# Optimization experiments

Hardware: AMD Instinct MI355X
Metric: run time of the kernel (lower is better)

## Reference

```python
import jax, jax.numpy as jnp
import numpy as np
import math

B, N, D, H = 32, 512, 512, 8
DK = D // H
MAX_DIST = 100.0
BINS = 20
BIN_SIZE = MAX_DIST / BINS


def setup_inputs() -> dict:
    key = jax.random.key(0)
    ks = jax.random.split(key, 12)
    s = 1.0 / math.sqrt(D)
    inp = {
        "x": jax.random.normal(ks[0], (B, N, D), dtype=jnp.float32),
        "distance_matrix": jax.random.uniform(ks[1], (B, N, N), dtype=jnp.float32) * MAX_DIST,
        "Wq": jax.random.uniform(ks[2], (D, D), jnp.float32, -s, s),
        "bq": jax.random.uniform(ks[3], (D,), jnp.float32, -s, s),
        "Wk": jax.random.uniform(ks[4], (D, D), jnp.float32, -s, s),
        "bk": jax.random.uniform(ks[5], (D,), jnp.float32, -s, s),
        "Wv": jax.random.uniform(ks[6], (D, D), jnp.float32, -s, s),
        "bv": jax.random.uniform(ks[7], (D,), jnp.float32, -s, s),
        "Wo": jax.random.uniform(ks[8], (D, D), jnp.float32, -s, s),
        "bo": jax.random.uniform(ks[9], (D,), jnp.float32, -s, s),
        "dist_weights": jnp.ones((BINS + 1,), dtype=jnp.float32),
    }
    return inp


def reference(x, distance_matrix, Wq, bq, Wk, bk, Wv, bv, Wo, bo, dist_weights):
    temperature = 1.0
    # Linear projections; torch nn.Linear computes x @ W.T + b
    q = (x @ Wq.T + bq).reshape(B, N, H, DK).transpose(0, 2, 1, 3)  # [B,H,N,DK]
    k = (x @ Wk.T + bk).reshape(B, N, H, DK).transpose(0, 2, 1, 3)
    v = (x @ Wv.T + bv).reshape(B, N, H, DK).transpose(0, 2, 1, 3)

    scores = jnp.einsum("bhqd,bhkd->bhqk", q, k) / math.sqrt(DK)  # [B,H,N,N]

    # Relative position bias: bin distances, look up scalar weight per pair
    binned = jnp.clip((distance_matrix / BIN_SIZE).astype(jnp.int32), 0, BINS)  # [B,N,N]
    bias = dist_weights[binned] / temperature  # [B,N,N]
    scores = scores + bias[:, None, :, :]  # broadcast over heads

    attn = jax.nn.softmax(scores, axis=-1)  # dropout is identity in eval
    out = jnp.einsum("bhqk,bhkd->bhqd", attn, v)  # [B,H,N,DK]
    out = out.transpose(0, 2, 1, 3).reshape(B, N, D)
    return out @ Wo.T + bo
```

## Files before the change

kernel.cpp:

```cpp
#include <hip/hip_runtime.h>
#include <hip/hip_fp16.h>
#include <math.h>
#include <stdint.h>

#define BB 32
#define NN 512
#define DDIM 512
#define HH 8
#define DK 64

typedef __attribute__((ext_vector_type(8))) short short8;
typedef __attribute__((ext_vector_type(8))) _Float16 half8;
typedef __attribute__((ext_vector_type(2))) _Float16 half2v;
typedef __attribute__((ext_vector_type(4))) float floatx4;
typedef __attribute__((ext_vector_type(16))) float floatx16;
typedef unsigned short ushort_t;
typedef unsigned int uint_t;

__device__ __forceinline__ void gl_lds16(const void* g, void* l) {
    __builtin_amdgcn_global_load_lds(
        (const __attribute__((address_space(1))) uint_t*)g,
        (__attribute__((address_space(3))) uint_t*)l,
        16, 0, 0);
}

__device__ __forceinline__ ushort_t f2bf(float f) {
    uint_t u = __builtin_bit_cast(uint_t, f);
    u += 0x7fff + ((u >> 16) & 1);
    return (ushort_t)(u >> 16);
}

__device__ __forceinline__ uint_t pkbf(float a, float b) {
    return (uint_t)f2bf(a) | ((uint_t)f2bf(b) << 16);
}

__device__ __forceinline__ uint_t pkh(float a, float b) {
    return __builtin_bit_cast(uint_t, __builtin_amdgcn_cvt_pkrtz(a, b));
}

__device__ __forceinline__ float h2f(ushort_t u) {
    return __half2float(__ushort_as_half(u));
}

__global__ __launch_bounds__(256) void cvt_bf16(const float* __restrict__ s,
                                                ushort_t* __restrict__ d, int n8) {
    const int i = blockIdx.x * 256 + threadIdx.x;
    if (i >= n8) return;
    const float4 a = ((const float4*)s)[i * 2 + 0];
    const float4 b = ((const float4*)s)[i * 2 + 1];
    uint4 o;
    o.x = pkbf(a.x, a.y); o.y = pkbf(a.z, a.w);
    o.z = pkbf(b.x, b.y); o.w = pkbf(b.z, b.w);
    *(uint4*)(d + i * 8) = o;
}

__global__ __launch_bounds__(256) void cvt_w4(
    const float* __restrict__ w0, const float* __restrict__ w1,
    const float* __restrict__ w2, const float* __restrict__ w3,
    ushort_t* __restrict__ o0, ushort_t* __restrict__ o1,
    ushort_t* __restrict__ o2, ushort_t* __restrict__ o3) {
    const float* s; ushort_t* d;
    if (blockIdx.y == 0)      { s = w0; d = o0; }
    else if (blockIdx.y == 1) { s = w1; d = o1; }
    else if (blockIdx.y == 2) { s = w2; d = o2; }
    else                      { s = w3; d = o3; }
    const int i = blockIdx.x * 256 + threadIdx.x;
    const float4 a = ((const float4*)s)[i * 2 + 0];
    const float4 b = ((const float4*)s)[i * 2 + 1];
    uint4 o;
    o.x = pkbf(a.x, a.y); o.y = pkbf(a.z, a.w);
    o.z = pkbf(b.x, b.y); o.w = pkbf(b.z, b.w);
    *(uint4*)(d + i * 8) = o;
}

__global__ __launch_bounds__(256) void bias_half(const float* __restrict__ dist,
                                                 const float* __restrict__ dw,
                                                 ushort_t* __restrict__ T, int n8) {
    __shared__ float dws[21];
    if (threadIdx.x < 21) dws[threadIdx.x] = (dw[threadIdx.x] - 3.0f) * 1.44269504f;
    __syncthreads();
    const int i = blockIdx.x * 256 + threadIdx.x;
    if (i >= n8) return;
    float dv[8];
    { const float4 a = ((const float4*)dist)[i * 2 + 0];
      const float4 b = ((const float4*)dist)[i * 2 + 1];
      dv[0]=a.x; dv[1]=a.y; dv[2]=a.z; dv[3]=a.w;
      dv[4]=b.x; dv[5]=b.y; dv[6]=b.z; dv[7]=b.w; }
    ushort_t h[8];
    #pragma unroll
    for (int j = 0; j < 8; ++j) {
        int bin = (int)(dv[j] / 5.0f);
        bin = bin < 0 ? 0 : (bin > 20 ? 20 : bin);
        h[j] = __half_as_ushort(__float2half(dws[bin]));
    }
    uint4 o;
    o.x = (uint_t)h[0] | ((uint_t)h[1] << 16);
    o.y = (uint_t)h[2] | ((uint_t)h[3] << 16);
    o.z = (uint_t)h[4] | ((uint_t)h[5] << 16);
    o.w = (uint_t)h[6] | ((uint_t)h[7] << 16);
    *(uint4*)(T + i * 8) = o;
}

__global__ __launch_bounds__(256) void transp_v(const ushort_t* __restrict__ V,
                                                ushort_t* __restrict__ Vt) {
    __shared__ ushort_t T[64][72];
    const int tid = threadIdx.x;
    const int q0 = blockIdx.x * 64;
    const int bh = blockIdx.y, b = bh >> 3, h = bh & 7;
    #pragma unroll
    for (int rnd = 0; rnd < 2; ++rnd) {
        const int idx = rnd * 256 + tid;
        const int row = idx >> 3, c8 = (idx & 7) * 8;
        const uint4 v = *(const uint4*)&V[((size_t)(b * NN + q0 + row)) * DDIM + h * DK + c8];
        ushort_t* t = &T[row][c8];
        t[0] = (ushort_t)v.x; t[1] = (ushort_t)(v.x >> 16);
        t[2] = (ushort_t)v.y; t[3] = (ushort_t)(v.y >> 16);
        t[4] = (ushort_t)v.z; t[5] = (ushort_t)(v.z >> 16);
        t[6] = (ushort_t)v.w; t[7] = (ushort_t)(v.w >> 16);
    }
    __syncthreads();
    #pragma unroll
    for (int rnd = 0; rnd < 2; ++rnd) {
        const int idx = rnd * 256 + tid;
        const int d = idx >> 3, q8 = (idx & 7) * 8;
        uint4 o;
        o.x = (uint_t)T[q8 + 0][d] | ((uint_t)T[q8 + 1][d] << 16);
        o.y = (uint_t)T[q8 + 2][d] | ((uint_t)T[q8 + 3][d] << 16);
        o.z = (uint_t)T[q8 + 4][d] | ((uint_t)T[q8 + 5][d] << 16);
        o.w = (uint_t)T[q8 + 6][d] | ((uint_t)T[q8 + 7][d] << 16);
        *(uint4*)&Vt[((size_t)(bh * DK + d)) * NN + q0 + q8] = o;
    }
}

#define GEMM_CORE(Aptr, Wptr)                                                           \
    __shared__ ushort_t As[128 * 32];                                                   \
    __shared__ ushort_t Bs[128 * 32];                                                   \
    const int tid = threadIdx.x;                                                        \
    const int lane = tid & 63, wid = tid >> 6;                                          \
    const int quad = lane >> 4, l15 = lane & 15;                                        \
    const int m0 = blockIdx.x * 128, n0 = blockIdx.y * 128;                             \
    const int wy = wid >> 1, wx = wid & 1;                                              \
    floatx4 acc[4][4];                                                                  \
    _Pragma("unroll") for (int i = 0; i < 4; ++i)                                       \
        _Pragma("unroll") for (int j = 0; j < 4; ++j)                                   \
            _Pragma("unroll") for (int r = 0; r < 4; ++r) acc[i][j][r] = 0.f;           \
    for (int k0 = 0; k0 < DDIM; k0 += 32) {                                             \
        __syncthreads();                                                                \
        _Pragma("unroll") for (int j = 0; j < 4; ++j) {                                 \
            const int t = wid * 4 + j;                                                  \
            const int rowi = ((t & 7) << 4) + (lane >> 2);                              \
            const int cd = (lane & 3) ^ ((rowi >> 1) & 3);                              \
            if (t < 8)                                                                  \
                gl_lds16(Aptr + (size_t)(m0 + rowi) * DDIM + k0 + cd * 8,               \
                         (char*)As + ((t & 7) << 10));                                  \
            else                                                                        \
                gl_lds16(Wptr + (size_t)(n0 + rowi) * DDIM + k0 + cd * 8,               \
                         (char*)Bs + ((t & 7) << 10));                                  \
        }                                                                               \
        __syncthreads();                                                                \
        short8 aw[4], bt[4];                                                            \
        _Pragma("unroll") for (int fi = 0; fi < 4; ++fi) {                              \
            const int r = wy * 64 + fi * 16 + l15;                                      \
            aw[fi] = *(const short8*)((const char*)Bs + r * 64 +                        \
                                      ((quad ^ ((r >> 1) & 3)) << 4));                  \
        }                                                                               \
        _Pragma("unroll") for (int ti = 0; ti < 4; ++ti) {                              \
            const int r = wx * 64 + ti * 16 + l15;                                      \
            bt[ti] = *(const short8*)((const char*)As + r * 64 +                        \
                                      ((quad ^ ((r >> 1) & 3)) << 4));                  \
        }                                                                               \
        _Pragma("unroll") for (int fi = 0; fi < 4; ++fi)                                \
            _Pragma("unroll") for (int ti = 0; ti < 4; ++ti)                            \
                acc[fi][ti] = __builtin_amdgcn_mfma_f32_16x16x32_bf16(                  \
                    aw[fi], bt[ti], acc[fi][ti], 0, 0, 0);                              \
    }

__global__ __launch_bounds__(256) void gemm_qkv(
    const ushort_t* __restrict__ A,
    const ushort_t* __restrict__ W0, const ushort_t* __restrict__ W1,
    const ushort_t* __restrict__ W2,
    const float* __restrict__ b0, const float* __restrict__ b1,
    const float* __restrict__ b2,
    ushort_t* __restrict__ o0, ushort_t* __restrict__ o1, ushort_t* __restrict__ o2) {
    const ushort_t* W; const float* bias; ushort_t* dst;
    if (blockIdx.z == 0)      { W = W0; bias = b0; dst = o0; }
    else if (blockIdx.z == 1) { W = W1; bias = b1; dst = o1; }
    else                      { W = W2; bias = b2; dst = o2; }
    const bool as_f16 = (blockIdx.z == 2);
    GEMM_CORE(A, W)
    #pragma unroll
    for (int fi = 0; fi < 4; ++fi) {
        const int f = n0 + wy * 64 + fi * 16 + quad * 4;
        const float4 b4 = *(const float4*)&bias[f];
        #pragma unroll
        for (int ti = 0; ti < 4; ++ti) {
            const int token = m0 + wx * 64 + ti * 16 + l15;
            const float v0 = acc[fi][ti][0] + b4.x, v1 = acc[fi][ti][1] + b4.y;
            const float v2 = acc[fi][ti][2] + b4.z, v3 = acc[fi][ti][3] + b4.w;
            uint2 v;
            if (as_f16) { v.x = pkh(v0, v1);  v.y = pkh(v2, v3); }
            else        { v.x = pkbf(v0, v1); v.y = pkbf(v2, v3); }
            *(uint2*)&dst[(size_t)token * DDIM + f] = v;
        }
    }
}

__global__ __launch_bounds__(256) void gemm_out(
    const ushort_t* __restrict__ A, const ushort_t* __restrict__ Wo,
    const float* __restrict__ bo, float* __restrict__ dst) {
    GEMM_CORE(A, Wo)
    #pragma unroll
    for (int fi = 0; fi < 4; ++fi) {
        const int f = n0 + wy * 64 + fi * 16 + quad * 4;
        const float4 b4 = *(const float4*)&bo[f];
        #pragma unroll
        for (int ti = 0; ti < 4; ++ti) {
            const int token = m0 + wx * 64 + ti * 16 + l15;
            float4 v;
            v.x = acc[fi][ti][0] + b4.x; v.y = acc[fi][ti][1] + b4.y;
            v.z = acc[fi][ti][2] + b4.z; v.w = acc[fi][ti][3] + b4.w;
            *(float4*)&dst[(size_t)token * DDIM + f] = v;
        }
    }
}

__global__ __launch_bounds__(512)
__attribute__((amdgpu_waves_per_eu(2, 2)))
void attn_fused(
    const ushort_t* __restrict__ Qg, const ushort_t* __restrict__ Kg,
    const ushort_t* __restrict__ Vtg, const ushort_t* __restrict__ Tg,
    ushort_t* __restrict__ aout) {
    __shared__ ushort_t Ks[512 * 64];
    __shared__ ushort_t Vs[64 * 512];

    const int tid = threadIdx.x, lane = tid & 63, wid = tid >> 6;
    const int l31 = lane & 31, hl = lane >> 5;
    const int h = blockIdx.x, b = blockIdx.y;
    const float K1 = 0.18033688f;

    #pragma unroll
    for (int j = 0; j < 8; ++j) {
        const int t = wid * 8 + j;
        {
            const int row = t * 8 + (lane >> 3);
            const int key = (row & 7) ^ ((row >> 3) & 7);
            const int g = (lane & 7) ^ key;
            gl_lds16(Kg + (size_t)(b * NN + row) * DDIM + h * DK + g * 8,
                     (char*)Ks + t * 1024);
        }
        {
            const int key = (t & 7) ^ ((t >> 3) & 7);
            const int g = lane ^ key;
            gl_lds16(Vtg + (size_t)((b * HH + h) * DK + t) * NN + g * 8,
                     (char*)Vs + t * 1024);
        }
    }

    short8 bq[2][4];
    #pragma unroll
    for (int qt = 0; qt < 2; ++qt) {
        const ushort_t* qp =
            Qg + (size_t)(b * NN + wid * 64 + qt * 32 + l31) * DDIM + h * DK + hl * 8;
        #pragma unroll
        for (int st = 0; st < 4; ++st) bq[qt][st] = *(const short8*)(qp + st * 16);
    }

    float lsum[2] = {0.f, 0.f};
    floatx16 O[2][2];
    #pragma unroll
    for (int qt = 0; qt < 2; ++qt)
        #pragma unroll
        for (int dt = 0; dt < 2; ++dt)
            #pragma unroll
            for (int r = 0; r < 16; ++r) O[qt][dt][r] = 0.f;

    __syncthreads();

    for (int kt = 0; kt < 8; ++kt) {
        uint2 tv[2][2][4];
        #pragma unroll
        for (int qt = 0; qt < 2; ++qt) {
            const ushort_t* tp =
                Tg + (size_t)(b * NN + wid * 64 + qt * 32 + l31) * NN + kt * 64 + hl * 4;
            #pragma unroll
            for (int kti = 0; kti < 2; ++kti)
                #pragma unroll
                for (int g = 0; g < 4; ++g)
                    tv[qt][kti][g] = *(const uint2*)(tp + kti * 32 + g * 8);
        }

        #pragma unroll
        for (int kti = 0; kti < 2; ++kti) {
            short8 kf[4];
            {
                const int row = kt * 64 + kti * 32 + l31;
                const int key = (row & 7) ^ ((row >> 3) & 7);
                #pragma unroll
                for (int st = 0; st < 4; ++st)
                    kf[st] = *(const short8*)((const char*)Ks + row * 128 +
                                              (((st * 2 + hl) ^ key) << 4));
            }
            half8 vf[2][2];
            #pragma unroll
            for (int dt = 0; dt < 2; ++dt) {
                const int d = dt * 32 + l31;
                const int key = (d & 7) ^ ((d >> 3) & 7);
                #pragma unroll
                for (int ks = 0; ks < 2; ++ks)
                    vf[dt][ks] = *(const half8*)((const char*)Vs + d * 1024 +
                        (((kt * 8 + kti * 4 + ks * 2 + hl) ^ key) << 4));
            }

            #pragma unroll
            for (int qt = 0; qt < 2; ++qt) {
                floatx16 S;
                #pragma unroll
                for (int r = 0; r < 16; ++r) S[r] = 0.f;
                __builtin_amdgcn_s_setprio(1);
                #pragma unroll
                for (int st = 0; st < 4; ++st)
                    S = __builtin_amdgcn_mfma_f32_32x32x16_bf16(
                        kf[st], bq[qt][st], S, 0, 0, 0);
                __builtin_amdgcn_s_setprio(0);

                float ls = 0.f;
                #pragma unroll
                for (int ks = 0; ks < 2; ++ks) {
                    float pp[8];
                    #pragma unroll
                    for (int gg = 0; gg < 2; ++gg) {
                        const uint2 tg = tv[qt][kti][ks * 2 + gg];
                        const float t0 = h2f((ushort_t)tg.x);
                        const float t1 = h2f((ushort_t)(tg.x >> 16));
                        const float t2 = h2f((ushort_t)tg.y);
                        const float t3 = h2f((ushort_t)(tg.y >> 16));
                        const int sb = ks * 8 + gg * 4;
                        pp[gg * 4 + 0] = exp2f(S[sb + 0] * K1 + t0);
                        pp[gg * 4 + 1] = exp2f(S[sb + 1] * K1 + t1);
                        pp[gg * 4 + 2] = exp2f(S[sb + 2] * K1 + t2);
                        pp[gg * 4 + 3] = exp2f(S[sb + 3] * K1 + t3);
                        ls += (pp[gg * 4 + 0] + pp[gg * 4 + 1]) +
                              (pp[gg * 4 + 2] + pp[gg * 4 + 3]);
                    }
                    uint_t w0 = pkh(pp[0], pp[1]);
                    uint_t w1 = pkh(pp[2], pp[3]);
                    uint_t w2 = pkh(pp[4], pp[5]);
                    uint_t w3 = pkh(pp[6], pp[7]);
                    auto r02 = __builtin_amdgcn_permlane32_swap(w0, w2, false, false);
                    auto r13 = __builtin_amdgcn_permlane32_swap(w1, w3, false, false);
                    uint4 uu;
                    uu.x = r02[0];
                    uu.y = r13[0];
                    uu.z = r02[1];
                    uu.w = r13[1];
                    const half8 bp = __builtin_bit_cast(half8, uu);

                    __builtin_amdgcn_s_setprio(1);
                    #pragma unroll
                    for (int dt = 0; dt < 2; ++dt)
                        O[qt][dt] = __builtin_amdgcn_mfma_f32_32x32x16_f16(
                            vf[dt][ks], bp, O[qt][dt], 0, 0, 0);
                    __builtin_amdgcn_s_setprio(0);
                }
                lsum[qt] += ls;
            }
        }
    }

    #pragma unroll
    for (int qt = 0; qt < 2; ++qt) {
        float l = lsum[qt];
        l += __shfl_xor(l, 32);
        const float inv = 1.0f / l;
        const size_t orow =
            (size_t)(b * NN + wid * 64 + qt * 32 + l31) * DDIM + h * DK;
        #pragma unroll
        for (int dt = 0; dt < 2; ++dt)
            #pragma unroll
            for (int g = 0; g < 4; ++g) {
                const int d = dt * 32 + g * 8 + hl * 4;
                uint2 ov;
                ov.x = pkbf(O[qt][dt][g * 4 + 0] * inv, O[qt][dt][g * 4 + 1] * inv);
                ov.y = pkbf(O[qt][dt][g * 4 + 2] * inv, O[qt][dt][g * 4 + 3] * inv);
                *(uint2*)&aout[orow + d] = ov;
            }
    }
}

extern "C" void kernel_launch(void* const* d_in, const int* in_sizes, int n_in,
                              void* d_out, int out_size, void* d_ws, size_t ws_size,
                              hipStream_t stream) {
    const float* x    = (const float*)d_in[0];
    const float* dist = (const float*)d_in[1];
    const float* Wq   = (const float*)d_in[2];
    const float* bq   = (const float*)d_in[3];
    const float* Wk   = (const float*)d_in[4];
    const float* bk   = (const float*)d_in[5];
    const float* Wv   = (const float*)d_in[6];
    const float* bv   = (const float*)d_in[7];
    const float* Wo   = (const float*)d_in[8];
    const float* bo   = (const float*)d_in[9];
    const float* dw   = (const float*)d_in[10];
    float* out = (float*)d_out;

    const size_t NELT = (size_t)BB * NN * DDIM;
    ushort_t* xb  = (ushort_t*)d_ws;
    ushort_t* wqb = xb + NELT;
    ushort_t* wkb = wqb + DDIM * DDIM;
    ushort_t* wvb = wkb + DDIM * DDIM;
    ushort_t* wob = wvb + DDIM * DDIM;
    ushort_t* qb  = wob + DDIM * DDIM;
    ushort_t* kb  = qb + NELT;
    ushort_t* vb  = kb + NELT;
    ushort_t* vt  = vb + NELT;
    ushort_t* Tm  = vt + NELT;
    ushort_t* ab  = xb;

    cvt_bf16<<<4096, 256, 0, stream>>>(x, xb, (int)(NELT / 8));
    cvt_w4<<<dim3(128, 4), 256, 0, stream>>>(Wq, Wk, Wv, Wo, wqb, wkb, wvb, wob);
    bias_half<<<4096, 256, 0, stream>>>(dist, dw, Tm, (int)(NELT / 8));

    gemm_qkv<<<dim3(128, 4, 3), 256, 0, stream>>>(xb, wqb, wkb, wvb, bq, bk, bv,
                                                  qb, kb, vb);
    transp_v<<<dim3(8, 256), 256, 0, stream>>>(vb, vt);
    attn_fused<<<dim3(HH, BB), 512, 0, stream>>>(qb, kb, vt, Tm, ab);
    gemm_out<<<dim3(128, 4), 256, 0, stream>>>(ab, wob, bo, out);
}
```

Measured before the change: 238.6 us.

## Double-buffer GEMM LDS tiles with K=64 steps and async prefetch

Rewrites the shared GEMM core to use two LDS buffers with a 64-wide K tile. The next tile is prefetched via global_load_lds while MFMAs consume the current one, with explicit vmcnt waits and raw barriers replacing syncthreads. It also changes the XOR swizzle and sets waves_per_eu to 2. This is meant to hide global-load latency in the QKV and output projections, at the cost of 4x LDS per block and reliance on hand-counted vmcnt values.

```diff
diff --git a/kernel.cpp b/kernel.cpp
--- a/kernel.cpp
+++ b/kernel.cpp
@@ -133,49 +133,68 @@
 }
 
 #define GEMM_CORE(Aptr, Wptr)                                                           \
-    __shared__ ushort_t As[128 * 32];                                                   \
-    __shared__ ushort_t Bs[128 * 32];                                                   \
+    __shared__ ushort_t As[2][128 * 64];                                                \
+    __shared__ ushort_t Bs[2][128 * 64];                                                \
     const int tid = threadIdx.x;                                                        \
     const int lane = tid & 63, wid = tid >> 6;                                          \
     const int quad = lane >> 4, l15 = lane & 15;                                        \
     const int m0 = blockIdx.x * 128, n0 = blockIdx.y * 128;                             \
     const int wy = wid >> 1, wx = wid & 1;                                              \
+    const int srow = lane >> 3, sg = lane & 7;                                          \
     floatx4 acc[4][4];                                                                  \
     _Pragma("unroll") for (int i = 0; i < 4; ++i)                                       \
         _Pragma("unroll") for (int j = 0; j < 4; ++j)                                   \
             _Pragma("unroll") for (int r = 0; r < 4; ++r) acc[i][j][r] = 0.f;           \
-    for (int k0 = 0; k0 < DDIM; k0 += 32) {                                             \
-        __syncthreads();                                                                \
-        _Pragma("unroll") for (int j = 0; j < 4; ++j) {                                 \
-            const int t = wid * 4 + j;                                                  \
-            const int rowi = ((t & 7) << 4) + (lane >> 2);                              \
-            const int cd = (lane & 3) ^ ((rowi >> 1) & 3);                              \
-            if (t < 8)                                                                  \
-                gl_lds16(Aptr + (size_t)(m0 + rowi) * DDIM + k0 + cd * 8,               \
-                         (char*)As + ((t & 7) << 10));                                  \
-            else                                                                        \
-                gl_lds16(Wptr + (size_t)(n0 + rowi) * DDIM + k0 + cd * 8,               \
-                         (char*)Bs + ((t & 7) << 10));                                  \
+    _Pragma("unroll") for (int j = 0; j < 4; ++j) {                                     \
+        const int t = wid * 4 + j;                                                      \
+        const int row = t * 8 + srow;                                                   \
+        const int g = sg ^ (row & 7);                                                   \
+        gl_lds16(Aptr + (size_t)(m0 + row) * DDIM + g * 8,                              \
+                 (char*)&As[0][0] + t * 1024);                                          \
+        gl_lds16(Wptr + (size_t)(n0 + row) * DDIM + g * 8,                              \
+                 (char*)&Bs[0][0] + t * 1024);                                          \
+    }                                                                                   \
+    _Pragma("unroll") for (int kt = 0; kt < 8; ++kt) {                                  \
+        const int cur = kt & 1;                                                         \
+        if (kt < 7) {                                                                   \
+            _Pragma("unroll") for (int j = 0; j < 4; ++j) {                             \
+                const int t = wid * 4 + j;                                              \
+                const int row = t * 8 + srow;                                           \
+                const int g = sg ^ (row & 7);                                           \
+                gl_lds16(Aptr + (size_t)(m0 + row) * DDIM + (kt + 1) * 64 + g * 8,      \
+                         (char*)&As[cur ^ 1][0] + t * 1024);                            \
+                gl_lds16(Wptr + (size_t)(n0 + row) * DDIM + (kt + 1) * 64 + g * 8,      \
+                         (char*)&Bs[cur ^ 1][0] + t * 1024);                            \
+            }                                                                           \
+            asm volatile("s_waitcnt vmcnt(8)" ::: "memory");                            \
+        } else {                                                                        \
+            asm volatile("s_waitcnt vmcnt(0)" ::: "memory");                            \
         }                                                                               \
-        __syncthreads();                                                                \
-        short8 aw[4], bt[4];                                                            \
-        _Pragma("unroll") for (int fi = 0; fi < 4; ++fi) {                              \
-            const int r = wy * 64 + fi * 16 + l15;                                      \
-            aw[fi] = *(const short8*)((const char*)Bs + r * 64 +                        \
-                                      ((quad ^ ((r >> 1) & 3)) << 4));                  \
+        __builtin_amdgcn_s_barrier();                                                   \
+        _Pragma("unroll") for (int h = 0; h < 2; ++h) {                                 \
+            short8 aw[4], bt[4];                                                        \
+            _Pragma("unroll") for (int fi = 0; fi < 4; ++fi) {                          \
+                const int r = wy * 64 + fi * 16 + l15;                                  \
+                aw[fi] = *(const short8*)((const char*)&Bs[cur][0] + r * 128 +          \
+                                          (((h * 4 + quad) ^ (r & 7)) << 4));           \
+            }                                                                           \
+            _Pragma("unroll") for (int ti = 0; ti < 4; ++ti) {                          \
+                const int r = wx * 64 + ti * 16 + l15;                                  \
+                bt[ti] = *(const short8*)((const char*)&As[cur][0] + r * 128 +          \
+                                          (((h * 4 + quad) ^ (r & 7)) << 4));           \
+            }                                                                           \
+            _Pragma("unroll") for (int fi = 0; fi < 4; ++fi)                            \
+                _Pragma("unroll") for (int ti = 0; ti < 4; ++ti)                        \
+                    acc[fi][ti] = __builtin_amdgcn_mfma_f32_16x16x32_bf16(              \
+                        aw[fi], bt[ti], acc[fi][ti], 0, 0, 0);                          \
         }                                                                               \
-        _Pragma("unroll") for (int ti = 0; ti < 4; ++ti) {                              \
-            const int r = wx * 64 + ti * 16 + l15;                                      \
-            bt[ti] = *(const short8*)((const char*)As + r * 64 +                        \
-                                      ((quad ^ ((r >> 1) & 3)) << 4));                  \
-        }                                                                               \
-        _Pragma("unroll") for (int fi = 0; fi < 4; ++fi)                                \
-            _Pragma("unroll") for (int ti = 0; ti < 4; ++ti)                            \
-                acc[fi][ti] = __builtin_amdgcn_mfma_f32_16x16x32_bf16(                  \
-                    aw[fi], bt[ti], acc[fi][ti], 0, 0, 0);                              \
-    }
-
-__global__ __launch_bounds__(256) void gemm_qkv(
+        asm volatile("" ::: "memory");                                                  \
+        __builtin_amdgcn_s_barrier();                                                   \
+    }
+
+__global__ __launch_bounds__(256)
+__attribute__((amdgpu_waves_per_eu(2, 2)))
+void gemm_qkv(
     const ushort_t* __restrict__ A,
     const ushort_t* __restrict__ W0, const ushort_t* __restrict__ W1,
     const ushort_t* __restrict__ W2,
@@ -205,7 +224,9 @@
     }
 }
 
-__global__ __launch_bounds__(256) void gemm_out(
+__global__ __launch_bounds__(256)
+__attribute__((amdgpu_waves_per_eu(2, 2)))
+void gemm_out(
     const ushort_t* __restrict__ A, const ushort_t* __restrict__ Wo,
     const float* __restrict__ bo, float* __restrict__ dst) {
     GEMM_CORE(A, Wo)
```

Measured after the change: 238.2 us. No clear change (-0.2%).

## Merge prep kernels into one launch and write V transposed from QKV GEMM

Applied to the files above, without the earlier changes.

The three conversion kernels (x to bf16, distance bias to fp16, four weight matrices to bf16) become one kernel that dispatches on block index, cutting launch count. The V projection epilogue now stores fp16 directly in the per-head transposed layout the attention kernel wants, which removes the separate transpose kernel and an intermediate buffer round-trip. The transposed stores are scalar 2-byte writes strided by NN, with consecutive lanes hitting consecutive q positions, so coalescing is partial and the epilogue may get slower.

```diff
diff --git a/kernel.cpp b/kernel.cpp
--- a/kernel.cpp
+++ b/kernel.cpp
@@ -11,7 +11,6 @@
 
 typedef __attribute__((ext_vector_type(8))) short short8;
 typedef __attribute__((ext_vector_type(8))) _Float16 half8;
-typedef __attribute__((ext_vector_type(2))) _Float16 half2v;
 typedef __attribute__((ext_vector_type(4))) float floatx4;
 typedef __attribute__((ext_vector_type(16))) float floatx16;
 typedef unsigned short ushort_t;
@@ -42,93 +41,61 @@
     return __half2float(__ushort_as_half(u));
 }
 
-__global__ __launch_bounds__(256) void cvt_bf16(const float* __restrict__ s,
-                                                ushort_t* __restrict__ d, int n8) {
-    const int i = blockIdx.x * 256 + threadIdx.x;
-    if (i >= n8) return;
-    const float4 a = ((const float4*)s)[i * 2 + 0];
-    const float4 b = ((const float4*)s)[i * 2 + 1];
-    uint4 o;
-    o.x = pkbf(a.x, a.y); o.y = pkbf(a.z, a.w);
-    o.z = pkbf(b.x, b.y); o.w = pkbf(b.z, b.w);
-    *(uint4*)(d + i * 8) = o;
-}
-
-__global__ __launch_bounds__(256) void cvt_w4(
-    const float* __restrict__ w0, const float* __restrict__ w1,
-    const float* __restrict__ w2, const float* __restrict__ w3,
-    ushort_t* __restrict__ o0, ushort_t* __restrict__ o1,
-    ushort_t* __restrict__ o2, ushort_t* __restrict__ o3) {
-    const float* s; ushort_t* d;
-    if (blockIdx.y == 0)      { s = w0; d = o0; }
-    else if (blockIdx.y == 1) { s = w1; d = o1; }
-    else if (blockIdx.y == 2) { s = w2; d = o2; }
-    else                      { s = w3; d = o3; }
-    const int i = blockIdx.x * 256 + threadIdx.x;
-    const float4 a = ((const float4*)s)[i * 2 + 0];
-    const float4 b = ((const float4*)s)[i * 2 + 1];
-    uint4 o;
-    o.x = pkbf(a.x, a.y); o.y = pkbf(a.z, a.w);
-    o.z = pkbf(b.x, b.y); o.w = pkbf(b.z, b.w);
-    *(uint4*)(d + i * 8) = o;
-}
-
-__global__ __launch_bounds__(256) void bias_half(const float* __restrict__ dist,
-                                                 const float* __restrict__ dw,
-                                                 ushort_t* __restrict__ T, int n8) {
-    __shared__ float dws[21];
-    if (threadIdx.x < 21) dws[threadIdx.x] = (dw[threadIdx.x] - 3.0f) * 1.44269504f;
-    __syncthreads();
-    const int i = blockIdx.x * 256 + threadIdx.x;
-    if (i >= n8) return;
-    float dv[8];
-    { const float4 a = ((const float4*)dist)[i * 2 + 0];
-      const float4 b = ((const float4*)dist)[i * 2 + 1];
-      dv[0]=a.x; dv[1]=a.y; dv[2]=a.z; dv[3]=a.w;
-      dv[4]=b.x; dv[5]=b.y; dv[6]=b.z; dv[7]=b.w; }
-    ushort_t h[8];
-    #pragma unroll
-    for (int j = 0; j < 8; ++j) {
-        int bin = (int)(dv[j] / 5.0f);
-        bin = bin < 0 ? 0 : (bin > 20 ? 20 : bin);
-        h[j] = __half_as_ushort(__float2half(dws[bin]));
-    }
-    uint4 o;
-    o.x = (uint_t)h[0] | ((uint_t)h[1] << 16);
-    o.y = (uint_t)h[2] | ((uint_t)h[3] << 16);
-    o.z = (uint_t)h[4] | ((uint_t)h[5] << 16);
-    o.w = (uint_t)h[6] | ((uint_t)h[7] << 16);
-    *(uint4*)(T + i * 8) = o;
-}
-
-__global__ __launch_bounds__(256) void transp_v(const ushort_t* __restrict__ V,
-                                                ushort_t* __restrict__ Vt) {
-    __shared__ ushort_t T[64][72];
-    const int tid = threadIdx.x;
-    const int q0 = blockIdx.x * 64;
-    const int bh = blockIdx.y, b = bh >> 3, h = bh & 7;
-    #pragma unroll
-    for (int rnd = 0; rnd < 2; ++rnd) {
-        const int idx = rnd * 256 + tid;
-        const int row = idx >> 3, c8 = (idx & 7) * 8;
-        const uint4 v = *(const uint4*)&V[((size_t)(b * NN + q0 + row)) * DDIM + h * DK + c8];
-        ushort_t* t = &T[row][c8];
-        t[0] = (ushort_t)v.x; t[1] = (ushort_t)(v.x >> 16);
-        t[2] = (ushort_t)v.y; t[3] = (ushort_t)(v.y >> 16);
-        t[4] = (ushort_t)v.z; t[5] = (ushort_t)(v.z >> 16);
-        t[6] = (ushort_t)v.w; t[7] = (ushort_t)(v.w >> 16);
-    }
-    __syncthreads();
-    #pragma unroll
-    for (int rnd = 0; rnd < 2; ++rnd) {
-        const int idx = rnd * 256 + tid;
-        const int d = idx >> 3, q8 = (idx & 7) * 8;
+__global__ __launch_bounds__(256) void prep_all(
+    const float* __restrict__ x, const float* __restrict__ dist,
+    const float* __restrict__ dw,
+    const float* __restrict__ Wq, const float* __restrict__ Wk,
+    const float* __restrict__ Wv, const float* __restrict__ Wo,
+    ushort_t* __restrict__ xb, ushort_t* __restrict__ Tm,
+    ushort_t* __restrict__ wqb, ushort_t* __restrict__ wkb,
+    ushort_t* __restrict__ wvb, ushort_t* __restrict__ wob) {
+    const int bx = blockIdx.x;
+    if (bx < 4096) {
+        const int i = bx * 256 + threadIdx.x;
+        const float4 a = ((const float4*)x)[i * 2 + 0];
+        const float4 b = ((const float4*)x)[i * 2 + 1];
         uint4 o;
-        o.x = (uint_t)T[q8 + 0][d] | ((uint_t)T[q8 + 1][d] << 16);
-        o.y = (uint_t)T[q8 + 2][d] | ((uint_t)T[q8 + 3][d] << 16);
-        o.z = (uint_t)T[q8 + 4][d] | ((uint_t)T[q8 + 5][d] << 16);
-        o.w = (uint_t)T[q8 + 6][d] | ((uint_t)T[q8 + 7][d] << 16);
-        *(uint4*)&Vt[((size_t)(bh * DK + d)) * NN + q0 + q8] = o;
+        o.x = pkbf(a.x, a.y); o.y = pkbf(a.z, a.w);
+        o.z = pkbf(b.x, b.y); o.w = pkbf(b.z, b.w);
+        *(uint4*)(xb + (size_t)i * 8) = o;
+    } else if (bx < 8192) {
+        __shared__ float dws[21];
+        if (threadIdx.x < 21) dws[threadIdx.x] = (dw[threadIdx.x] - 3.0f) * 1.44269504f;
+        __syncthreads();
+        const int i = (bx - 4096) * 256 + threadIdx.x;
+        float dv[8];
+        { const float4 a = ((const float4*)dist)[i * 2 + 0];
+          const float4 b = ((const float4*)dist)[i * 2 + 1];
+          dv[0]=a.x; dv[1]=a.y; dv[2]=a.z; dv[3]=a.w;
+          dv[4]=b.x; dv[5]=b.y; dv[6]=b.z; dv[7]=b.w; }
+        ushort_t h[8];
+        #pragma unroll
+        for (int j = 0; j < 8; ++j) {
+            int bin = (int)(dv[j] / 5.0f);
+            bin = bin < 0 ? 0 : (bin > 20 ? 20 : bin);
+            h[j] = __half_as_ushort(__float2half(dws[bin]));
+        }
+        uint4 o;
+        o.x = (uint_t)h[0] | ((uint_t)h[1] << 16);
+        o.y = (uint_t)h[2] | ((uint_t)h[3] << 16);
+        o.z = (uint_t)h[4] | ((uint_t)h[5] << 16);
+        o.w = (uint_t)h[6] | ((uint_t)h[7] << 16);
+        *(uint4*)(Tm + (size_t)i * 8) = o;
+    } else {
+        const int bw = bx - 8192;
+        const int w = bw >> 7;
+        const float* s; ushort_t* d;
+        if (w == 0)      { s = Wq; d = wqb; }
+        else if (w == 1) { s = Wk; d = wkb; }
+        else if (w == 2) { s = Wv; d = wvb; }
+        else             { s = Wo; d = wob; }
+        const int i = (bw & 127) * 256 + threadIdx.x;
+        const float4 a = ((const float4*)s)[i * 2 + 0];
+        const float4 b = ((const float4*)s)[i * 2 + 1];
+        uint4 o;
+        o.x = pkbf(a.x, a.y); o.y = pkbf(a.z, a.w);
+        o.z = pkbf(b.x, b.y); o.w = pkbf(b.z, b.w);
+        *(uint4*)(d + (size_t)i * 8) = o;
     }
 }
 
@@ -188,19 +155,42 @@
     else                      { W = W2; bias = b2; dst = o2; }
     const bool as_f16 = (blockIdx.z == 2);
     GEMM_CORE(A, W)
-    #pragma unroll
-    for (int fi = 0; fi < 4; ++fi) {
-        const int f = n0 + wy * 64 + fi * 16 + quad * 4;
-        const float4 b4 = *(const float4*)&bias[f];
-        #pragma unroll
-        for (int ti = 0; ti < 4; ++ti) {
-            const int token = m0 + wx * 64 + ti * 16 + l15;
-            const float v0 = acc[fi][ti][0] + b4.x, v1 = acc[fi][ti][1] + b4.y;
-            const float v2 = acc[fi][ti][2] + b4.z, v3 = acc[fi][ti][3] + b4.w;
-            uint2 v;
-            if (as_f16) { v.x = pkh(v0, v1);  v.y = pkh(v2, v3); }
-            else        { v.x = pkbf(v0, v1); v.y = pkbf(v2, v3); }
-            *(uint2*)&dst[(size_t)token * DDIM + f] = v;
+    if (as_f16) {
+        const int hh = (n0 + wy * 64) >> 6;
+        const size_t vrow0 = ((size_t)((m0 >> 9) * HH + hh)) * DK;
+        const int q0 = (m0 & 511) + wx * 64;
+        #pragma unroll
+        for (int fi = 0; fi < 4; ++fi) {
+            const int f = n0 + wy * 64 + fi * 16 + quad * 4;
+            const float4 b4 = *(const float4*)&bias[f];
+            const int d = fi * 16 + quad * 4;
+            #pragma unroll
+            for (int ti = 0; ti < 4; ++ti) {
+                const int q = q0 + ti * 16 + l15;
+                dst[(vrow0 + d + 0) * NN + q] =
+                    __half_as_ushort(__float2half(acc[fi][ti][0] + b4.x));
+                dst[(vrow0 + d + 1) * NN + q] =
+                    __half_as_ushort(__float2half(acc[fi][ti][1] + b4.y));
+                dst[(vrow0 + d + 2) * NN + q] =
+                    __half_as_ushort(__float2half(acc[fi][ti][2] + b4.z));
+                dst[(vrow0 + d + 3) * NN + q] =
+                    __half_as_ushort(__float2half(acc[fi][ti][3] + b4.w));
+            }
+        }
+    } else {
+        #pragma unroll
+        for (int fi = 0; fi < 4; ++fi) {
+            const int f = n0 + wy * 64 + fi * 16 + quad * 4;
+            const float4 b4 = *(const float4*)&bias[f];
+            #pragma unroll
+            for (int ti = 0; ti < 4; ++ti) {
+                const int token = m0 + wx * 64 + ti * 16 + l15;
+                const float v0 = acc[fi][ti][0] + b4.x, v1 = acc[fi][ti][1] + b4.y;
+                const float v2 = acc[fi][ti][2] + b4.z, v3 = acc[fi][ti][3] + b4.w;
+                uint2 v;
+                v.x = pkbf(v0, v1); v.y = pkbf(v2, v3);
+                *(uint2*)&dst[(size_t)token * DDIM + f] = v;
+            }
         }
     }
 }
@@ -411,18 +401,14 @@
     ushort_t* wob = wvb + DDIM * DDIM;
     ushort_t* qb  = wob + DDIM * DDIM;
     ushort_t* kb  = qb + NELT;
-    ushort_t* vb  = kb + NELT;
-    ushort_t* vt  = vb + NELT;
+    ushort_t* vt  = kb + NELT;
     ushort_t* Tm  = vt + NELT;
     ushort_t* ab  = xb;
 
-    cvt_bf16<<<4096, 256, 0, stream>>>(x, xb, (int)(NELT / 8));
-    cvt_w4<<<dim3(128, 4), 256, 0, stream>>>(Wq, Wk, Wv, Wo, wqb, wkb, wvb, wob);
-    bias_half<<<4096, 256, 0, stream>>>(dist, dw, Tm, (int)(NELT / 8));
-
+    prep_all<<<8704, 256, 0, stream>>>(x, dist, dw, Wq, Wk, Wv, Wo,
+                                       xb, Tm, wqb, wkb, wvb, wob);
     gemm_qkv<<<dim3(128, 4, 3), 256, 0, stream>>>(xb, wqb, wkb, wvb, bq, bk, bv,
-                                                  qb, kb, vb);
-    transp_v<<<dim3(8, 256), 256, 0, stream>>>(vb, vt);
+                                                  qb, kb, vt);
     attn_fused<<<dim3(HH, BB), 512, 0, stream>>>(qb, kb, vt, Tm, ab);
     gemm_out<<<dim3(128, 4), 256, 0, stream>>>(ab, wob, bo, out);
 }
```

Result: faster. 231.8 us (-2.9%).
